# Kernel tuning notes

Hardware: AMD Instinct MI355X
Metric: run time of the kernel (lower is better)

## Reference

```python
import jax, jax.numpy as jnp
import numpy as np
import math

SL, BS, D, NH, PF, STRIDE, LAYERS = 2048, 4, 512, 8, 3, 1, 1
DH = D // NH
N_SPF = 9  # 0-2: hidden (a,t,v cross-attend to raw inputs); 3-5: cross (at,tv,va, shared for reverse dir); 6-8: self
EMBED_SCALE = math.sqrt(D)


def _ln(x, g, b):
    m = x.mean(-1, keepdims=True)
    var = ((x - m) ** 2).mean(-1, keepdims=True)
    return (x - m) / jnp.sqrt(var + 1e-5) * g + b


def _sinusoid(sl, d):
    half = d // 2
    inv = jnp.exp(jnp.arange(half, dtype=jnp.float32) * (-math.log(10000.0) / (half - 1)))
    ang = jnp.arange(sl, dtype=jnp.float32)[:, None] * inv[None, :]
    return jnp.concatenate([jnp.sin(ang), jnp.cos(ang)], axis=-1)  # (sl, d)


def setup_inputs() -> dict:
    key = jax.random.key(0)
    ks = jax.random.split(key, 16)
    s = 0.02
    p = {}
    p['a'] = jax.random.normal(ks[0], (SL, BS, D), jnp.float32)
    p['t'] = jax.random.normal(ks[1], (SL, BS, D), jnp.float32)
    p['v'] = jax.random.normal(ks[2], (SL, BS, D), jnp.float32)
    p['init_hiddens'] = s * jax.random.normal(ks[3], (3, D), jnp.float32)
    # stacked MultiheadAttention weights for the 9 SPF blocks
    p['wq'] = s * jax.random.normal(ks[4], (N_SPF, D, D), jnp.float32)
    p['bq'] = jnp.zeros((N_SPF, D), jnp.float32)
    p['wk'] = s * jax.random.normal(ks[5], (N_SPF, D, D), jnp.float32)
    p['bk'] = jnp.zeros((N_SPF, D), jnp.float32)
    p['wv'] = s * jax.random.normal(ks[6], (N_SPF, D, D), jnp.float32)
    p['bv'] = jnp.zeros((N_SPF, D), jnp.float32)
    p['wo'] = s * jax.random.normal(ks[7], (N_SPF, D, D), jnp.float32)
    p['bo'] = jnp.zeros((N_SPF, D), jnp.float32)
    p['ln_g'] = jnp.ones((N_SPF, D), jnp.float32)
    p['ln_b'] = jnp.zeros((N_SPF, D), jnp.float32)
    p['lnkv_g'] = jnp.ones((N_SPF, D), jnp.float32)
    p['lnkv_b'] = jnp.zeros((N_SPF, D), jnp.float32)
    # stacked FFN weights for the 9 FFN blocks
    p['w1'] = s * jax.random.normal(ks[8], (N_SPF, 4 * D, D), jnp.float32)
    p['b1'] = jnp.zeros((N_SPF, 4 * D), jnp.float32)
    p['w2'] = s * jax.random.normal(ks[9], (N_SPF, D, 4 * D), jnp.float32)
    p['b2'] = jnp.zeros((N_SPF, D), jnp.float32)
    p['fln_g'] = jnp.ones((N_SPF, D), jnp.float32)
    p['fln_b'] = jnp.zeros((N_SPF, D), jnp.float32)
    p['out_g'] = jnp.ones((D,), jnp.float32)
    p['out_b'] = jnp.zeros((D,), jnp.float32)
    return p


def reference(a, t, v, init_hiddens, wq, bq, wk, bk, wv, bv, wo, bo,
              ln_g, ln_b, lnkv_g, lnkv_b, w1, b1, w2, b2, fln_g, fln_b,
              out_g, out_b):
    scale = DH ** -0.5
    # precomputed strided modulo gather indices: r[i,j] = (i+1)*stride - pf + j
    idx = ((jnp.arange(SL) + 1) * STRIDE - PF)[:, None] + jnp.arange(PF)[None, :]  # (SL, PF)

    def spf(i, x, ctx, has_kv):
        # x: (SL, BS, D); ctx: (CL, BS, D) or None (self-attention on normed x)
        res = x
        xn = _ln(x, ln_g[i], ln_b[i])
        c = xn if ctx is None else ctx
        kv = c[idx % c.shape[0]]                      # (SL, PF, BS, D) modulo-gathered window
        if has_kv:
            kv = _ln(kv, lnkv_g[i], lnkv_b[i])
        q = (xn @ wq[i].T + bq[i]).reshape(SL, BS, NH, DH) * scale
        k = (kv @ wk[i].T + bk[i]).reshape(SL, PF, BS, NH, DH)
        vv = (kv @ wv[i].T + bv[i]).reshape(SL, PF, BS, NH, DH)
        attn = jax.nn.softmax(jnp.einsum('sbnd,spbnd->sbnp', q, k), axis=-1)
        o = jnp.einsum('sbnp,spbnd->sbnd', attn, vv).reshape(SL, BS, D)
        return res + o @ wo[i].T + bo[i]

    def ffn(i, x):
        h = jax.nn.relu(_ln(x, fln_g[i], fln_b[i]) @ w1[i].T + b1[i])
        return x + h @ w2[i].T + b2[i]

    pos = _sinusoid(SL, D)[:, None, :]
    a = a * EMBED_SCALE + pos
    t = t * EMBED_SCALE + pos
    v = v * EMBED_SCALE + pos
    h_a = jnp.broadcast_to(init_hiddens[0], (SL, BS, D))
    h_t = jnp.broadcast_to(init_hiddens[1], (SL, BS, D))
    h_v = jnp.broadcast_to(init_hiddens[2], (SL, BS, D))

    for _ in range(LAYERS):
        # hidden layer: hiddens cross-attend to raw modality streams
        h_a = ffn(0, spf(0, h_a, a, True))
        h_t = ffn(1, spf(1, h_t, t, True))
        h_v = ffn(2, spf(2, h_v, v, True))
        # cross layer: six branches, three shared weight sets (forward/reverse)
        h_at = ffn(3, spf(3, h_a, h_t, True))
        h_tv = ffn(4, spf(4, h_t, h_v, True))
        h_va = ffn(5, spf(5, h_v, h_a, True))
        h_ta = ffn(3, spf(3, h_t, h_a, True))
        h_vt = ffn(4, spf(4, h_v, h_t, True))
        h_av = ffn(5, spf(5, h_a, h_v, True))
        h_a, h_t, h_v = h_at + h_av, h_ta + h_tv, h_va + h_vt
        # self layer
        h_a = ffn(6, spf(6, h_a, None, False))
        h_t = ffn(7, spf(7, h_t, None, False))
        h_v = ffn(8, spf(8, h_v, None, False))

    return jnp.stack([_ln(h_a, out_g, out_b), _ln(h_t, out_g, out_b), _ln(h_v, out_g, out_b)])
```

## Files before the change

### kernel.cpp

```cpp
#include <hip/hip_runtime.h>

#define SL 2048
#define BS 4
#define DM 512
#define NH 8
#define DH 64
#define RD 8192
#define DF 2048

#define BM 128
#define BN 128
#define BK 32

typedef unsigned short u16;
typedef __attribute__((ext_vector_type(8))) short short8;
typedef __attribute__((ext_vector_type(4))) float f32x4;

__device__ __forceinline__ float bf2f(u16 u) {
  return __uint_as_float(((unsigned)u) << 16);
}
__device__ __forceinline__ u16 f2bf(float f) {
  unsigned u = __float_as_uint(f);
  unsigned r = (u + 0x7fffu + ((u >> 16) & 1u)) >> 16;
  return (u16)r;
}

typedef __attribute__((address_space(3))) unsigned int lds_u32;
typedef __attribute__((address_space(1))) unsigned int gbl_u32;
__device__ __forceinline__ void gload_lds16(const void* g, void* l) {
  __builtin_amdgcn_global_load_lds((gbl_u32*)g, (lds_u32*)l, 16, 0, 0);
}

struct GemmDesc {
  const u16* A;
  const u16* B;
  const float* bias;
  const float* res;
  u16* Cb;
  float* Cf;
  float bmul;
  int relu;
};
struct GemmBatch { GemmDesc d[9]; };

struct LnDesc { const float* x; const float* g; const float* b; u16* yb; float* yf; };
struct LnBatch { LnDesc d[6]; };

struct AttnDesc { const u16* Q; const u16* K; const u16* V; u16* O; };
struct AttnBatch { AttnDesc d[3]; };

struct CvtDesc { const float* src; u16* dst; int n8; float scale; };
struct CvtBatch { CvtDesc d[6]; };

struct EmbBatch { const float* src[3]; float* dst[3]; const float* pos; };
struct AddBatch { const float* a[3]; const float* b[3]; float* o[3]; };

__global__ __launch_bounds__(256) void gemm_k(GemmBatch args, int M, int N, int K) {
  GemmDesc g = args.d[blockIdx.z];
  __shared__ u16 As[BM * BK];
  __shared__ u16 Ws[BN * BK];
  const int t = threadIdx.x;
  const int w = t >> 6, l = t & 63;
  const int mb = blockIdx.y, nb = blockIdx.x;
  const u16* Ag = g.A + (size_t)mb * BM * K;
  const u16* Wg = g.B + (size_t)nb * BN * K;
  f32x4 acc[4][4];
#pragma unroll
  for (int m = 0; m < 4; ++m)
#pragma unroll
    for (int n = 0; n < 4; ++n) acc[m][n] = f32x4{0.f, 0.f, 0.f, 0.f};
  const int wr = (w >> 1) * 64, wc = (w & 1) * 64;
  const int lr = l & 15, lk = (l >> 4) * 8;

  for (int k0 = 0; k0 < K; k0 += BK) {
    if (k0) __syncthreads();
#pragma unroll
    for (int i = 0; i < 2; ++i) {
      const int u = (i << 8) + t;
      const int row = u >> 2, col = (u & 3) << 3;
      gload_lds16(Ag + (size_t)row * K + k0 + col, (char*)As + (i << 12) + (w << 10));
      gload_lds16(Wg + (size_t)row * K + k0 + col, (char*)Ws + (i << 12) + (w << 10));
    }
    __syncthreads();
    short8 af[4], bfr[4];
#pragma unroll
    for (int m = 0; m < 4; ++m)
      af[m] = *(const short8*)(As + (wr + m * 16 + lr) * BK + lk);
#pragma unroll
    for (int n = 0; n < 4; ++n)
      bfr[n] = *(const short8*)(Ws + (wc + n * 16 + lr) * BK + lk);
#pragma unroll
    for (int m = 0; m < 4; ++m)
#pragma unroll
      for (int n = 0; n < 4; ++n)
        acc[m][n] = __builtin_amdgcn_mfma_f32_16x16x32_bf16(af[m], bfr[n], acc[m][n], 0, 0, 0);
  }

  const int c0 = nb * BN + wc + lr;
  const int r0 = mb * BM + wr + (l >> 4) * 4;
#pragma unroll
  for (int n = 0; n < 4; ++n) {
    const int gc = c0 + n * 16;
    const float bi = g.bias ? g.bias[gc] * g.bmul : 0.f;
#pragma unroll
    for (int m = 0; m < 4; ++m) {
#pragma unroll
      for (int r = 0; r < 4; ++r) {
        const size_t off = (size_t)(r0 + m * 16 + r) * N + gc;
        float v = acc[m][n][r] + bi;
        if (g.res) v += g.res[off];
        if (g.relu) v = fmaxf(v, 0.f);
        if (g.Cb) g.Cb[off] = f2bf(v);
        else g.Cf[off] = v;
      }
    }
  }
}

__global__ __launch_bounds__(256) void ln_k(LnBatch args) {
  LnDesc d = args.d[blockIdx.y];
  const int row = blockIdx.x * 4 + (threadIdx.x >> 6);
  const int l = threadIdx.x & 63;
  const float* xp = d.x + (size_t)row * DM + l * 8;
  float4 x0 = *(const float4*)xp;
  float4 x1 = *(const float4*)(xp + 4);
  float xv[8] = {x0.x, x0.y, x0.z, x0.w, x1.x, x1.y, x1.z, x1.w};
  float s = 0.f, ss = 0.f;
#pragma unroll
  for (int j = 0; j < 8; ++j) { s += xv[j]; ss += xv[j] * xv[j]; }
#pragma unroll
  for (int m = 1; m < 64; m <<= 1) {
    s += __shfl_xor(s, m, 64);
    ss += __shfl_xor(ss, m, 64);
  }
  const float mean = s * (1.f / DM);
  const float var = ss * (1.f / DM) - mean * mean;
  const float rstd = rsqrtf(var + 1e-5f);
  float4 g0 = *(const float4*)(d.g + l * 8);
  float4 g1 = *(const float4*)(d.g + l * 8 + 4);
  float4 b0 = *(const float4*)(d.b + l * 8);
  float4 b1 = *(const float4*)(d.b + l * 8 + 4);
  float gv[8] = {g0.x, g0.y, g0.z, g0.w, g1.x, g1.y, g1.z, g1.w};
  float bv[8] = {b0.x, b0.y, b0.z, b0.w, b1.x, b1.y, b1.z, b1.w};
  float y[8];
#pragma unroll
  for (int j = 0; j < 8; ++j) y[j] = (xv[j] - mean) * rstd * gv[j] + bv[j];
  if (d.yb) {
    short8 p;
#pragma unroll
    for (int j = 0; j < 8; ++j) p[j] = (short)f2bf(y[j]);
    *(short8*)(d.yb + (size_t)row * DM + l * 8) = p;
  } else {
    float* o = d.yf + (size_t)row * DM + l * 8;
    *(float4*)o = float4{y[0], y[1], y[2], y[3]};
    *(float4*)(o + 4) = float4{y[4], y[5], y[6], y[7]};
  }
}

__global__ __launch_bounds__(256) void attn_k(AttnBatch args) {
  AttnDesc d = args.d[blockIdx.y];
  const int idx = blockIdx.x * 256 + threadIdx.x;
  const int h = idx & 7;
  const int b = (idx >> 3) & 3;
  const int s = idx >> 5;
  const int s0 = (s + SL - 2) & (SL - 1);
  const int s1 = (s + SL - 1) & (SL - 1);
  const size_t rq = (size_t)(s * BS + b) * DM + h * DH;
  const size_t r0 = (size_t)(s0 * BS + b) * DM + h * DH;
  const size_t r1 = (size_t)(s1 * BS + b) * DM + h * DH;
  float d0 = 0.f, d1 = 0.f, d2 = 0.f;
#pragma unroll
  for (int c = 0; c < 8; ++c) {
    short8 q8 = *(const short8*)(d.Q + rq + c * 8);
    short8 k0 = *(const short8*)(d.K + r0 + c * 8);
    short8 k1 = *(const short8*)(d.K + r1 + c * 8);
    short8 k2 = *(const short8*)(d.K + rq + c * 8);
#pragma unroll
    for (int e = 0; e < 8; ++e) {
      const float q = bf2f((u16)q8[e]);
      d0 += q * bf2f((u16)k0[e]);
      d1 += q * bf2f((u16)k1[e]);
      d2 += q * bf2f((u16)k2[e]);
    }
  }
  const float mx = fmaxf(d0, fmaxf(d1, d2));
  float e0 = expf(d0 - mx), e1 = expf(d1 - mx), e2 = expf(d2 - mx);
  const float inv = 1.f / (e0 + e1 + e2);
  e0 *= inv; e1 *= inv; e2 *= inv;
#pragma unroll
  for (int c = 0; c < 8; ++c) {
    short8 v0 = *(const short8*)(d.V + r0 + c * 8);
    short8 v1 = *(const short8*)(d.V + r1 + c * 8);
    short8 v2 = *(const short8*)(d.V + rq + c * 8);
    short8 o8;
#pragma unroll
    for (int e = 0; e < 8; ++e)
      o8[e] = (short)f2bf(e0 * bf2f((u16)v0[e]) + e1 * bf2f((u16)v1[e]) + e2 * bf2f((u16)v2[e]));
    *(short8*)(d.O + rq + c * 8) = o8;
  }
}

__global__ __launch_bounds__(256) void cvt_k(CvtBatch a) {
  CvtDesc d = a.d[blockIdx.y];
  const int stride = gridDim.x * 256;
  for (int i = blockIdx.x * 256 + threadIdx.x; i < d.n8; i += stride) {
    float4 x0 = ((const float4*)d.src)[i * 2];
    float4 x1 = ((const float4*)d.src)[i * 2 + 1];
    short8 r;
    r[0] = (short)f2bf(x0.x * d.scale); r[1] = (short)f2bf(x0.y * d.scale);
    r[2] = (short)f2bf(x0.z * d.scale); r[3] = (short)f2bf(x0.w * d.scale);
    r[4] = (short)f2bf(x1.x * d.scale); r[5] = (short)f2bf(x1.y * d.scale);
    r[6] = (short)f2bf(x1.z * d.scale); r[7] = (short)f2bf(x1.w * d.scale);
    *(short8*)(d.dst + (size_t)i * 8) = r;
  }
}

__global__ __launch_bounds__(256) void pos_k(float* pos) {
  const int i = blockIdx.x * 256 + threadIdx.x;
  const int dd = i & (DM - 1);
  const int s = i >> 9;
  const int j = (dd < 256) ? dd : dd - 256;
  const float inv = expf((float)j * -0.036119374f);
  const float ang = (float)s * inv;
  pos[i] = (dd < 256) ? sinf(ang) : cosf(ang);
}

__global__ __launch_bounds__(256) void embed_k(EmbBatch a) {
  const int z = blockIdx.y;
  const int i = blockIdx.x * 256 + threadIdx.x;
  float4 x = ((const float4*)a.src[z])[i];
  const int e = i << 2;
  const int dcol = e & (DM - 1);
  const int srow = e >> 11;
  float4 p = *(const float4*)(a.pos + (size_t)srow * DM + dcol);
  const float SC = 22.627417f;
  float4 y{x.x * SC + p.x, x.y * SC + p.y, x.z * SC + p.z, x.w * SC + p.w};
  ((float4*)a.dst[z])[i] = y;
}

__global__ __launch_bounds__(256) void hinit_k(const float* init, float* H) {
  const int z = blockIdx.y;
  const int i = blockIdx.x * 256 + threadIdx.x;
  float4 w = ((const float4*)(init + z * DM))[i & 127];
  ((float4*)(H + (size_t)z * RD * DM))[i] = w;
}

__global__ __launch_bounds__(256) void add_k(AddBatch a) {
  const int z = blockIdx.y;
  const int i = blockIdx.x * 256 + threadIdx.x;
  float4 x = ((const float4*)a.a[z])[i];
  float4 y = ((const float4*)a.b[z])[i];
  float4 o{x.x + y.x, x.y + y.y, x.z + y.z, x.w + y.w};
  ((float4*)a.o[z])[i] = o;
}

extern "C" void kernel_launch(void* const* d_in, const int* in_sizes, int n_in,
                              void* d_out, int out_size, void* d_ws, size_t ws_size,
                              hipStream_t stream) {
  (void)in_sizes; (void)n_in; (void)out_size;
  const float* in_a  = (const float*)d_in[0];
  const float* in_t  = (const float*)d_in[1];
  const float* in_v  = (const float*)d_in[2];
  const float* initH = (const float*)d_in[3];
  const float* wq = (const float*)d_in[4];
  const float* bq = (const float*)d_in[5];
  const float* wk = (const float*)d_in[6];
  const float* bk = (const float*)d_in[7];
  const float* wv = (const float*)d_in[8];
  const float* bv = (const float*)d_in[9];
  const float* wo = (const float*)d_in[10];
  const float* bo = (const float*)d_in[11];
  const float* ln_g = (const float*)d_in[12];
  const float* ln_b = (const float*)d_in[13];
  const float* lnkv_g = (const float*)d_in[14];
  const float* lnkv_b = (const float*)d_in[15];
  const float* w1 = (const float*)d_in[16];
  const float* b1 = (const float*)d_in[17];
  const float* w2 = (const float*)d_in[18];
  const float* b2 = (const float*)d_in[19];
  const float* fln_g = (const float*)d_in[20];
  const float* fln_b = (const float*)d_in[21];
  const float* out_g = (const float*)d_in[22];
  const float* out_b = (const float*)d_in[23];
  float* out = (float*)d_out;

  char* ws = (char*)d_ws;
  u16* wq_b = (u16*)(ws + 0);
  u16* wk_b = (u16*)(ws + 4718592);
  u16* wv_b = (u16*)(ws + 9437184);
  u16* wo_b = (u16*)(ws + 14155776);
  u16* w1_b = (u16*)(ws + 18874368);
  u16* w2_b = (u16*)(ws + 37748736);
  const size_t slotF = (size_t)RD * DM * 4;
  const size_t slotB = (size_t)RD * DM * 2;
  const size_t oH = 56623104;
  const size_t oS = oH + 3 * slotF;
  const size_t oX = oS + 6 * slotF;
  const int G = (ws_size >= oX + 18 * slotB) ? 3 : 1;

  float* Hs[3]; float* Ss[6];
  for (int j = 0; j < 3; ++j) Hs[j] = (float*)(ws + oH + j * slotF);
  for (int i = 0; i < 6; ++i) Ss[i] = (float*)(ws + oS + i * slotF);
  auto XN = [&](int j) { return (u16*)(ws + oX + (size_t)j * slotB); };
  auto KN = [&](int j) { return (u16*)(ws + oX + (size_t)(G + j) * slotB); };
  auto QS = [&](int j) { return (u16*)(ws + oX + (size_t)(2 * G + 3 * j) * slotB); };
  auto KS = [&](int j) { return (u16*)(ws + oX + (size_t)(2 * G + 3 * j + 1) * slotB); };
  auto VS = [&](int j) { return (u16*)(ws + oX + (size_t)(2 * G + 3 * j + 2) * slotB); };
  auto F1 = [&](int j) { return (u16*)(ws + oX + (size_t)(2 * G + 4 * j) * slotB); };

  {
    CvtBatch cb{};
    cb.d[0] = CvtDesc{wq, wq_b, 294912, 0.125f};
    cb.d[1] = CvtDesc{wk, wk_b, 294912, 1.f};
    cb.d[2] = CvtDesc{wv, wv_b, 294912, 1.f};
    cb.d[3] = CvtDesc{wo, wo_b, 294912, 1.f};
    cb.d[4] = CvtDesc{w1, w1_b, 1179648, 1.f};
    cb.d[5] = CvtDesc{w2, w2_b, 1179648, 1.f};
    cvt_k<<<dim3(512, 6), 256, 0, stream>>>(cb);
  }
  float* pos = (float*)(ws + oX);
  pos_k<<<dim3(4096), 256, 0, stream>>>(pos);
  {
    EmbBatch eb{};
    eb.src[0] = in_a; eb.src[1] = in_t; eb.src[2] = in_v;
    eb.dst[0] = Ss[3]; eb.dst[1] = Ss[4]; eb.dst[2] = Ss[5];
    eb.pos = pos;
    embed_k<<<dim3(4096, 3), 256, 0, stream>>>(eb);
  }
  hinit_k<<<dim3(4096, 3), 256, 0, stream>>>(initH, (float*)(ws + oH));

  auto run_group = [&](int g, const int* xi, float* const* ctx, const int* wi,
                       float* const* sout, float* const* fout) {
    const bool self = (ctx == nullptr);
    {
      LnBatch lb{}; int nd = 0;
      for (int j = 0; j < g; ++j)
        lb.d[nd++] = LnDesc{Hs[xi[j]], ln_g + wi[j] * DM, ln_b + wi[j] * DM, XN(j), nullptr};
      if (!self)
        for (int j = 0; j < g; ++j)
          lb.d[nd++] = LnDesc{ctx[j], lnkv_g + wi[j] * DM, lnkv_b + wi[j] * DM, KN(j), nullptr};
      ln_k<<<dim3(2048, nd), 256, 0, stream>>>(lb);
    }
    {
      GemmBatch gb{}; int nd = 0;
      for (int j = 0; j < g; ++j)
        gb.d[nd++] = GemmDesc{XN(j), wq_b + (size_t)wi[j] * DM * DM, bq + wi[j] * DM,
                              nullptr, QS(j), nullptr, 0.125f, 0};
      for (int j = 0; j < g; ++j)
        gb.d[nd++] = GemmDesc{self ? XN(j) : KN(j), wk_b + (size_t)wi[j] * DM * DM, bk + wi[j] * DM,
                              nullptr, KS(j), nullptr, 1.f, 0};
      for (int j = 0; j < g; ++j)
        gb.d[nd++] = GemmDesc{self ? XN(j) : KN(j), wv_b + (size_t)wi[j] * DM * DM, bv + wi[j] * DM,
                              nullptr, VS(j), nullptr, 1.f, 0};
      gemm_k<<<dim3(DM / BN, RD / BM, nd), 256, 0, stream>>>(gb, RD, DM, DM);
    }
    {
      AttnBatch ab{};
      for (int j = 0; j < g; ++j) ab.d[j] = AttnDesc{QS(j), KS(j), VS(j), XN(j)};
      attn_k<<<dim3(256, g), 256, 0, stream>>>(ab);
    }
    {
      GemmBatch gb{};
      for (int j = 0; j < g; ++j)
        gb.d[j] = GemmDesc{XN(j), wo_b + (size_t)wi[j] * DM * DM, bo + wi[j] * DM,
                           Hs[xi[j]], nullptr, sout[j], 1.f, 0};
      gemm_k<<<dim3(DM / BN, RD / BM, g), 256, 0, stream>>>(gb, RD, DM, DM);
    }
    {
      LnBatch lb{};
      for (int j = 0; j < g; ++j)
        lb.d[j] = LnDesc{sout[j], fln_g + wi[j] * DM, fln_b + wi[j] * DM, KN(j), nullptr};
      ln_k<<<dim3(2048, g), 256, 0, stream>>>(lb);
    }
    {
      GemmBatch gb{};
      for (int j = 0; j < g; ++j)
        gb.d[j] = GemmDesc{KN(j), w1_b + (size_t)wi[j] * DF * DM, b1 + wi[j] * DF,
                           nullptr, F1(j), nullptr, 1.f, 1};
      gemm_k<<<dim3(DF / BN, RD / BM, g), 256, 0, stream>>>(gb, RD, DF, DM);
    }
    {
      GemmBatch gb{};
      for (int j = 0; j < g; ++j)
        gb.d[j] = GemmDesc{F1(j), w2_b + (size_t)wi[j] * DF * DM, b2 + wi[j] * DM,
                           sout[j], nullptr, fout[j], 1.f, 0};
      gemm_k<<<dim3(DM / BN, RD / BM, g), 256, 0, stream>>>(gb, RD, DM, DF);
    }
  };

  {
    const int xi[3] = {0, 1, 2}, wi[3] = {0, 1, 2};
    float* ctx[3] = {Ss[3], Ss[4], Ss[5]};
    float* sout[3] = {Ss[0], Ss[1], Ss[2]};
    float* fout[3] = {Hs[0], Hs[1], Hs[2]};
    for (int base = 0; base < 3; base += G) {
      const int g = (G < 3 - base) ? G : 3 - base;
      run_group(g, xi + base, ctx + base, wi + base, sout + base, fout + base);
    }
  }
  {
    const int xi[6] = {0, 1, 2, 1, 2, 0};
    const int ci[6] = {1, 2, 0, 0, 1, 2};
    const int wi[6] = {3, 4, 5, 3, 4, 5};
    float* ctx[6]; float* sout[6];
    for (int i = 0; i < 6; ++i) { ctx[i] = Hs[ci[i]]; sout[i] = Ss[i]; }
    for (int base = 0; base < 6; base += G) {
      const int g = (G < 6 - base) ? G : 6 - base;
      run_group(g, xi + base, ctx + base, wi + base, sout + base, sout + base);
    }
  }
  {
    AddBatch ab{};
    ab.a[0] = Ss[0]; ab.b[0] = Ss[5]; ab.o[0] = Hs[0];
    ab.a[1] = Ss[3]; ab.b[1] = Ss[1]; ab.o[1] = Hs[1];
    ab.a[2] = Ss[2]; ab.b[2] = Ss[4]; ab.o[2] = Hs[2];
    add_k<<<dim3(4096, 3), 256, 0, stream>>>(ab);
  }
  {
    const int xi[3] = {0, 1, 2}, wi[3] = {6, 7, 8};
    float* sout[3] = {Ss[0], Ss[1], Ss[2]};
    for (int base = 0; base < 3; base += G) {
      const int g = (G < 3 - base) ? G : 3 - base;
      run_group(g, xi + base, nullptr, wi + base, sout + base, sout + base);
    }
  }
  {
    LnBatch lb{};
    for (int j = 0; j < 3; ++j)
      lb.d[j] = LnDesc{Ss[j], out_g, out_b, nullptr, out + (size_t)j * RD * DM};
    ln_k<<<dim3(2048, 3), 256, 0, stream>>>(lb);
  }
}
```

Before: 2.709 ms.

## Double-buffer GEMM with swizzled LDS, narrower N tiles, fuse cross-branch add into FFN2

The GEMM kernel is templated on the N tile width and uses 64-wide tiles for the N=512 projections, which gives more blocks for better occupancy. It double-buffers the LDS stages so the next K slice loads while the MFMAs run. An XOR swizzle on the LDS column placement is meant to reduce bank conflicts. The separate add kernel is removed: the reverse cross branches accumulate into the forward outputs inside the FFN2 epilogue via a new accum flag, which saves one full read/write pass. Workspace slot assignment is reorganized so a G=2 batching path is possible, at the cost of more complex buffer aliasing.

```diff
diff --git a/kernel.cpp b/kernel.cpp
--- a/kernel.cpp
+++ b/kernel.cpp
@@ -9,7 +9,6 @@
 #define DF 2048
 
 #define BM 128
-#define BN 128
 #define BK 32
 
 typedef unsigned short u16;
@@ -40,6 +39,7 @@
   float* Cf;
   float bmul;
   int relu;
+  int accum;
 };
 struct GemmBatch { GemmDesc d[9]; };
 
@@ -53,53 +53,74 @@
 struct CvtBatch { CvtDesc d[6]; };
 
 struct EmbBatch { const float* src[3]; float* dst[3]; const float* pos; };
-struct AddBatch { const float* a[3]; const float* b[3]; float* o[3]; };
-
-__global__ __launch_bounds__(256) void gemm_k(GemmBatch args, int M, int N, int K) {
+
+template<int TBN>
+__global__ __launch_bounds__(256) void gemm_k(GemmBatch args, int N, int K) {
+  constexpr int NFR = TBN / 32;
+  constexpr int BU = TBN / 64;
   GemmDesc g = args.d[blockIdx.z];
-  __shared__ u16 As[BM * BK];
-  __shared__ u16 Ws[BN * BK];
+  __shared__ u16 As[2][BM * BK];
+  __shared__ u16 Bs[2][TBN * BK];
   const int t = threadIdx.x;
   const int w = t >> 6, l = t & 63;
-  const int mb = blockIdx.y, nb = blockIdx.x;
-  const u16* Ag = g.A + (size_t)mb * BM * K;
-  const u16* Wg = g.B + (size_t)nb * BN * K;
-  f32x4 acc[4][4];
+  const u16* Ag = g.A + (size_t)blockIdx.y * BM * K;
+  const u16* Bg = g.B + (size_t)blockIdx.x * TBN * K;
+  f32x4 acc[4][NFR];
 #pragma unroll
   for (int m = 0; m < 4; ++m)
 #pragma unroll
-    for (int n = 0; n < 4; ++n) acc[m][n] = f32x4{0.f, 0.f, 0.f, 0.f};
-  const int wr = (w >> 1) * 64, wc = (w & 1) * 64;
-  const int lr = l & 15, lk = (l >> 4) * 8;
-
-  for (int k0 = 0; k0 < K; k0 += BK) {
-    if (k0) __syncthreads();
+    for (int n = 0; n < NFR; ++n) acc[m][n] = f32x4{0.f, 0.f, 0.f, 0.f};
+  const int wr = (w >> 1) * 64;
+  const int wc = (w & 1) * (TBN / 2);
+  const int lr = l & 15;
+  const int cxo = ((l >> 4) ^ (l & 3)) << 3;
+
+  auto stage = [&](int buf, int k0) {
 #pragma unroll
     for (int i = 0; i < 2; ++i) {
       const int u = (i << 8) + t;
-      const int row = u >> 2, col = (u & 3) << 3;
-      gload_lds16(Ag + (size_t)row * K + k0 + col, (char*)As + (i << 12) + (w << 10));
-      gload_lds16(Wg + (size_t)row * K + k0 + col, (char*)Ws + (i << 12) + (w << 10));
-    }
+      const int row = u >> 2;
+      const int c = (u & 3) ^ (row & 3);
+      gload_lds16(Ag + (size_t)row * K + k0 + (c << 3),
+                  (char*)&As[buf][0] + (i << 12) + (w << 10));
+    }
+#pragma unroll
+    for (int i = 0; i < BU; ++i) {
+      const int u = (i << 8) + t;
+      const int row = u >> 2;
+      const int c = (u & 3) ^ (row & 3);
+      gload_lds16(Bg + (size_t)row * K + k0 + (c << 3),
+                  (char*)&Bs[buf][0] + (i << 12) + (w << 10));
+    }
+  };
+
+  stage(0, 0);
+  const int nt = K / BK;
+  int cur = 0;
+  for (int it = 0; it < nt; ++it) {
     __syncthreads();
-    short8 af[4], bfr[4];
+    if (it + 1 < nt) stage(cur ^ 1, (it + 1) * BK);
+    const u16* Ab = &As[cur][0];
+    const u16* Bb = &Bs[cur][0];
+    short8 af[4], bfr[NFR];
 #pragma unroll
     for (int m = 0; m < 4; ++m)
-      af[m] = *(const short8*)(As + (wr + m * 16 + lr) * BK + lk);
-#pragma unroll
-    for (int n = 0; n < 4; ++n)
-      bfr[n] = *(const short8*)(Ws + (wc + n * 16 + lr) * BK + lk);
+      af[m] = *(const short8*)(Ab + (wr + m * 16 + lr) * BK + cxo);
+#pragma unroll
+    for (int n = 0; n < NFR; ++n)
+      bfr[n] = *(const short8*)(Bb + (wc + n * 16 + lr) * BK + cxo);
 #pragma unroll
     for (int m = 0; m < 4; ++m)
 #pragma unroll
-      for (int n = 0; n < 4; ++n)
+      for (int n = 0; n < NFR; ++n)
         acc[m][n] = __builtin_amdgcn_mfma_f32_16x16x32_bf16(af[m], bfr[n], acc[m][n], 0, 0, 0);
-  }
-
-  const int c0 = nb * BN + wc + lr;
-  const int r0 = mb * BM + wr + (l >> 4) * 4;
-#pragma unroll
-  for (int n = 0; n < 4; ++n) {
+    cur ^= 1;
+  }
+
+  const int c0 = blockIdx.x * TBN + wc + lr;
+  const int r0 = blockIdx.y * BM + wr + ((l >> 4) << 2);
+#pragma unroll
+  for (int n = 0; n < NFR; ++n) {
     const int gc = c0 + n * 16;
     const float bi = g.bias ? g.bias[gc] * g.bmul : 0.f;
 #pragma unroll
@@ -110,8 +131,12 @@
         float v = acc[m][n][r] + bi;
         if (g.res) v += g.res[off];
         if (g.relu) v = fmaxf(v, 0.f);
-        if (g.Cb) g.Cb[off] = f2bf(v);
-        else g.Cf[off] = v;
+        if (g.Cb) {
+          g.Cb[off] = f2bf(v);
+        } else {
+          if (g.accum) v += g.Cf[off];
+          g.Cf[off] = v;
+        }
       }
     }
   }
@@ -243,15 +268,6 @@
   const int i = blockIdx.x * 256 + threadIdx.x;
   float4 w = ((const float4*)(init + z * DM))[i & 127];
   ((float4*)(H + (size_t)z * RD * DM))[i] = w;
-}
-
-__global__ __launch_bounds__(256) void add_k(AddBatch a) {
-  const int z = blockIdx.y;
-  const int i = blockIdx.x * 256 + threadIdx.x;
-  float4 x = ((const float4*)a.a[z])[i];
-  float4 y = ((const float4*)a.b[z])[i];
-  float4 o{x.x + y.x, x.y + y.y, x.z + y.z, x.w + y.w};
-  ((float4*)a.o[z])[i] = o;
 }
 
 extern "C" void kernel_launch(void* const* d_in, const int* in_sizes, int n_in,
@@ -296,17 +312,20 @@
   const size_t oH = 56623104;
   const size_t oS = oH + 3 * slotF;
   const size_t oX = oS + 6 * slotF;
-  const int G = (ws_size >= oX + 18 * slotB) ? 3 : 1;
+  int G = 1;
+  if (ws_size >= oX + 15 * slotB) G = 3;
+  else if (ws_size >= oX + 10 * slotB) G = 2;
 
   float* Hs[3]; float* Ss[6];
   for (int j = 0; j < 3; ++j) Hs[j] = (float*)(ws + oH + j * slotF);
   for (int i = 0; i < 6; ++i) Ss[i] = (float*)(ws + oS + i * slotF);
-  auto XN = [&](int j) { return (u16*)(ws + oX + (size_t)j * slotB); };
-  auto KN = [&](int j) { return (u16*)(ws + oX + (size_t)(G + j) * slotB); };
-  auto QS = [&](int j) { return (u16*)(ws + oX + (size_t)(2 * G + 3 * j) * slotB); };
-  auto KS = [&](int j) { return (u16*)(ws + oX + (size_t)(2 * G + 3 * j + 1) * slotB); };
-  auto VS = [&](int j) { return (u16*)(ws + oX + (size_t)(2 * G + 3 * j + 2) * slotB); };
-  auto F1 = [&](int j) { return (u16*)(ws + oX + (size_t)(2 * G + 4 * j) * slotB); };
+  auto SLOT = [&](int j) { return (u16*)(ws + oX + (size_t)j * slotB); };
+  auto KN = [&](int j) { return SLOT(j); };
+  auto XN = [&](int j) { return SLOT(G + j); };
+  auto QS = [&](int j) { return SLOT(2 * G + 3 * j); };
+  auto KS = [&](int j) { return SLOT(2 * G + 3 * j + 1); };
+  auto VS = [&](int j) { return SLOT(2 * G + 3 * j + 2); };
+  auto F1 = [&](int j) { return SLOT(G + 4 * j); };
 
   {
     CvtBatch cb{};
@@ -329,14 +348,13 @@
   }
   hinit_k<<<dim3(4096, 3), 256, 0, stream>>>(initH, (float*)(ws + oH));
 
-  auto run_group = [&](int g, const int* xi, float* const* ctx, const int* wi,
-                       float* const* sout, float* const* fout) {
-    const bool self = (ctx == nullptr);
+  auto run_group = [&](int g, float* const* xv, float* const* ctx, const int* wi,
+                       float* const* sout, float* const* fout, int accum) {
     {
       LnBatch lb{}; int nd = 0;
       for (int j = 0; j < g; ++j)
-        lb.d[nd++] = LnDesc{Hs[xi[j]], ln_g + wi[j] * DM, ln_b + wi[j] * DM, XN(j), nullptr};
-      if (!self)
+        lb.d[nd++] = LnDesc{xv[j], ln_g + wi[j] * DM, ln_b + wi[j] * DM, XN(j), nullptr};
+      if (ctx)
         for (int j = 0; j < g; ++j)
           lb.d[nd++] = LnDesc{ctx[j], lnkv_g + wi[j] * DM, lnkv_b + wi[j] * DM, KN(j), nullptr};
       ln_k<<<dim3(2048, nd), 256, 0, stream>>>(lb);
@@ -345,14 +363,14 @@
       GemmBatch gb{}; int nd = 0;
       for (int j = 0; j < g; ++j)
         gb.d[nd++] = GemmDesc{XN(j), wq_b + (size_t)wi[j] * DM * DM, bq + wi[j] * DM,
-                              nullptr, QS(j), nullptr, 0.125f, 0};
-      for (int j = 0; j < g; ++j)
-        gb.d[nd++] = GemmDesc{self ? XN(j) : KN(j), wk_b + (size_t)wi[j] * DM * DM, bk + wi[j] * DM,
-                              nullptr, KS(j), nullptr, 1.f, 0};
-      for (int j = 0; j < g; ++j)
-        gb.d[nd++] = GemmDesc{self ? XN(j) : KN(j), wv_b + (size_t)wi[j] * DM * DM, bv + wi[j] * DM,
-                              nullptr, VS(j), nullptr, 1.f, 0};
-      gemm_k<<<dim3(DM / BN, RD / BM, nd), 256, 0, stream>>>(gb, RD, DM, DM);
+                              nullptr, QS(j), nullptr, 0.125f, 0, 0};
+      for (int j = 0; j < g; ++j)
+        gb.d[nd++] = GemmDesc{ctx ? KN(j) : XN(j), wk_b + (size_t)wi[j] * DM * DM, bk + wi[j] * DM,
+                              nullptr, KS(j), nullptr, 1.f, 0, 0};
+      for (int j = 0; j < g; ++j)
+        gb.d[nd++] = GemmDesc{ctx ? KN(j) : XN(j), wv_b + (size_t)wi[j] * DM * DM, bv + wi[j] * DM,
+                              nullptr, VS(j), nullptr, 1.f, 0, 0};
+      gemm_k<64><<<dim3(DM / 64, RD / BM, nd), 256, 0, stream>>>(gb, DM, DM);
     }
     {
       AttnBatch ab{};
@@ -363,8 +381,8 @@
       GemmBatch gb{};
       for (int j = 0; j < g; ++j)
         gb.d[j] = GemmDesc{XN(j), wo_b + (size_t)wi[j] * DM * DM, bo + wi[j] * DM,
-                           Hs[xi[j]], nullptr, sout[j], 1.f, 0};
-      gemm_k<<<dim3(DM / BN, RD / BM, g), 256, 0, stream>>>(gb, RD, DM, DM);
+                           xv[j], nullptr, sout[j], 1.f, 0, 0};
+      gemm_k<64><<<dim3(DM / 64, RD / BM, g), 256, 0, stream>>>(gb, DM, DM);
     }
     {
       LnBatch lb{};
@@ -376,58 +394,60 @@
       GemmBatch gb{};
       for (int j = 0; j < g; ++j)
         gb.d[j] = GemmDesc{KN(j), w1_b + (size_t)wi[j] * DF * DM, b1 + wi[j] * DF,
-                           nullptr, F1(j), nullptr, 1.f, 1};
-      gemm_k<<<dim3(DF / BN, RD / BM, g), 256, 0, stream>>>(gb, RD, DF, DM);
+                           nullptr, F1(j), nullptr, 1.f, 1, 0};
+      gemm_k<128><<<dim3(DF / 128, RD / BM, g), 256, 0, stream>>>(gb, DF, DM);
     }
     {
       GemmBatch gb{};
       for (int j = 0; j < g; ++j)
-        gb.d[j] = GemmDesc{F1(j), w2_b + (size_t)wi[j] * DF * DM, b2 + wi[j] * DM,
-                           sout[j], nullptr, fout[j], 1.f, 0};
-      gemm_k<<<dim3(DM / BN, RD / BM, g), 256, 0, stream>>>(gb, RD, DM, DF);
+        gb.d[j] = GemmDesc{F1(j), w2_b + (size_t)wi[j] * DM * DF, b2 + wi[j] * DM,
+                           sout[j], nullptr, fout[j], 1.f, 0, accum};
+      gemm_k<64><<<dim3(DM / 64, RD / BM, g), 256, 0, stream>>>(gb, DM, DF);
     }
   };
 
-  {
-    const int xi[3] = {0, 1, 2}, wi[3] = {0, 1, 2};
+  auto drive = [&](int n, float* const* xv, float* const* ctx, const int* wi,
+                   float* const* sout, float* const* fout, int accum) {
+    for (int b = 0; b < n; b += G) {
+      const int g = (G < n - b) ? G : n - b;
+      run_group(g, xv + b, ctx ? ctx + b : nullptr, wi + b, sout + b, fout + b, accum);
+    }
+  };
+
+  {
+    float* xv[3] = {Hs[0], Hs[1], Hs[2]};
     float* ctx[3] = {Ss[3], Ss[4], Ss[5]};
+    const int wi[3] = {0, 1, 2};
     float* sout[3] = {Ss[0], Ss[1], Ss[2]};
     float* fout[3] = {Hs[0], Hs[1], Hs[2]};
-    for (int base = 0; base < 3; base += G) {
-      const int g = (G < 3 - base) ? G : 3 - base;
-      run_group(g, xi + base, ctx + base, wi + base, sout + base, fout + base);
-    }
-  }
-  {
-    const int xi[6] = {0, 1, 2, 1, 2, 0};
-    const int ci[6] = {1, 2, 0, 0, 1, 2};
-    const int wi[6] = {3, 4, 5, 3, 4, 5};
-    float* ctx[6]; float* sout[6];
-    for (int i = 0; i < 6; ++i) { ctx[i] = Hs[ci[i]]; sout[i] = Ss[i]; }
-    for (int base = 0; base < 6; base += G) {
-      const int g = (G < 6 - base) ? G : 6 - base;
-      run_group(g, xi + base, ctx + base, wi + base, sout + base, sout + base);
-    }
-  }
-  {
-    AddBatch ab{};
-    ab.a[0] = Ss[0]; ab.b[0] = Ss[5]; ab.o[0] = Hs[0];
-    ab.a[1] = Ss[3]; ab.b[1] = Ss[1]; ab.o[1] = Hs[1];
-    ab.a[2] = Ss[2]; ab.b[2] = Ss[4]; ab.o[2] = Hs[2];
-    add_k<<<dim3(4096, 3), 256, 0, stream>>>(ab);
-  }
-  {
-    const int xi[3] = {0, 1, 2}, wi[3] = {6, 7, 8};
+    drive(3, xv, ctx, wi, sout, fout, 0);
+  }
+  {
+    float* xv[3] = {Hs[0], Hs[1], Hs[2]};
+    float* ctx[3] = {Hs[1], Hs[2], Hs[0]};
+    const int wi[3] = {3, 4, 5};
     float* sout[3] = {Ss[0], Ss[1], Ss[2]};
-    for (int base = 0; base < 3; base += G) {
-      const int g = (G < 3 - base) ? G : 3 - base;
-      run_group(g, xi + base, nullptr, wi + base, sout + base, sout + base);
-    }
+    drive(3, xv, ctx, wi, sout, sout, 0);
+  }
+  {
+    float* xv[3] = {Hs[1], Hs[2], Hs[0]};
+    float* ctx[3] = {Hs[0], Hs[1], Hs[2]};
+    const int wi[3] = {3, 4, 5};
+    float* sout[3] = {Ss[3], Ss[4], Ss[5]};
+    float* fout[3] = {Ss[1], Ss[2], Ss[0]};
+    drive(3, xv, ctx, wi, sout, fout, 1);
+  }
+  {
+    float* xv[3] = {Ss[0], Ss[1], Ss[2]};
+    const int wi[3] = {6, 7, 8};
+    float* sout[3] = {Ss[3], Ss[4], Ss[5]};
+    float* fout[3] = {Hs[0], Hs[1], Hs[2]};
+    drive(3, xv, nullptr, wi, sout, fout, 0);
   }
   {
     LnBatch lb{};
     for (int j = 0; j < 3; ++j)
-      lb.d[j] = LnDesc{Ss[j], out_g, out_b, nullptr, out + (size_t)j * RD * DM};
+      lb.d[j] = LnDesc{Hs[j], out_g, out_b, nullptr, out + (size_t)j * RD * DM};
     ln_k<<<dim3(2048, 3), 256, 0, stream>>>(lb);
   }
 }
```

Result: faster. 2.454 ms (-9.4%).
